# Kernel optimization log

Measured on AMD Instinct MI355X. Metric: run time of the kernel, lower is better.

The kernel has to match this reference:

```python
import jax, jax.numpy as jnp
import numpy as np

PROPAGATION_RANGE = 2
PROP_OUT = PROPAGATION_RANGE - 1  # propagation_out_range


def setup_inputs() -> dict:
    key = jax.random.key(0)
    k1, k2 = jax.random.split(key)
    B, D, H, W = 2, 48, 512, 640
    neighbors = 9
    depth_min = jnp.full((B,), 425.0, dtype=jnp.float32)
    depth_max = jnp.full((B,), 935.0, dtype=jnp.float32)
    # depth samples uniformly inside [depth_min, depth_max]
    u = jax.random.uniform(k1, (B, D, H, W), dtype=jnp.float32)
    depth_sample = depth_min[:, None, None, None] + u * (depth_max - depth_min)[:, None, None, None]
    # per-neighbor weights (2*neighbors channels: far-range then near-range)
    offset = jax.random.uniform(k2, (B, 2 * neighbors, H, W), dtype=jnp.float32) / neighbors
    return {
        "depth_sample": depth_sample,
        "depth_min": depth_min,
        "depth_max": depth_max,
        "offset": offset,
        "patchmatch_interval_scale": 0.025,
        "evaluate_neighbors": neighbors,
    }


def reference(depth_sample, depth_min, depth_max, offset, patchmatch_interval_scale, evaluate_neighbors):
    neighbors = int(evaluate_neighbors)
    B, D, H, W = depth_sample.shape
    k = int(np.sqrt(neighbors))  # square neighborhood side

    # normalized inverse depth in [0, 1]
    inv_min = 1.0 / depth_min  # [B]
    inv_max = 1.0 / depth_max  # [B]
    x = (1.0 / depth_sample - inv_max[:, None, None, None]) / (inv_min - inv_max)[:, None, None, None]

    pad = k // 2 + PROP_OUT
    pad1 = 2 * pad
    xp = jnp.pad(x, ((0, 0), (0, 0), (pad, pad), (pad, pad)), mode="reflect")
    xp1 = jnp.pad(x, ((0, 0), (0, 0), (pad1, pad1), (pad1, pad1)), mode="reflect")

    step = PROP_OUT + 1
    acc = jnp.zeros_like(x)
    for s in range(neighbors):  # small static loop (9 neighbors)
        iy, ix = (s // k) * step, (s % k) * step
        iy1, ix1 = 2 * iy, 2 * ix
        # offset channel broadcasts over the depth dimension
        f1 = offset[:, s, None] * xp1[:, :, iy1:H + iy1, ix1:W + ix1]
        f = offset[:, s + neighbors, None] * xp[:, :, iy:H + iy, ix:W + ix]
        acc = acc + (f + f1) * 0.5

    x1 = jnp.abs(acc - x) / patchmatch_interval_scale
    x1 = jnp.clip(x1, 0.0, 4.0)
    return jax.nn.sigmoid((2.0 - x1) * 2.0)
```

## Files before the change

### kernel.cpp

```cpp
#include <hip/hip_runtime.h>

constexpr int Bc = 2, Dc = 48, Hc = 512, Wc = 640;
constexpr int HWc = Hc * Wc;

constexpr int TW = 32, TH = 16, NT = 256;
constexpr int NXT = Wc / TW;
constexpr int NYT = Hc / TH;
constexpr int NBLK = NXT * NYT * Bc;
constexpr int NXCD = 8;
constexpr int BPX = NBLK / NXCD;
constexpr int HALO = 4;
constexpr int SW = TW + 2 * HALO;
constexpr int SH = TH + 2 * HALO;
constexpr int PLANE = SW * SH;
constexpr int DC = 4;
constexpr int NIT = Dc / DC;
constexpr int NVEC = DC * PLANE / 4;
constexpr int VPT = (NVEC + NT - 1) / NT;
constexpr int NSC = DC * PLANE;
constexpr int SPT = NSC / NT;

__device__ __forceinline__ int reflect_h(int h) {
    return h < 0 ? -h : (h >= Hc ? 2 * (Hc - 1) - h : h);
}
__device__ __forceinline__ int reflect_w(int w) {
    return w < 0 ? -w : (w >= Wc ? 2 * (Wc - 1) - w : w);
}

__global__ __launch_bounds__(NT) void dw_kernel(
    const float* __restrict__ ds, const float* __restrict__ dmin,
    const float* __restrict__ dmax, const float* __restrict__ off,
    const float* __restrict__ scale_p, float* __restrict__ out)
{
    __shared__ float sx[2][DC * PLANE];

    const int hw  = blockIdx.x;
    const int l   = (hw & (NXCD - 1)) * BPX + (hw >> 3);
    const int bx  = l % NXT;
    const int rem = l / NXT;
    const int by  = rem % NYT;
    const int b   = rem / NYT;
    const int h0  = by * TH;
    const int w0  = bx * TW;
    const int tid = threadIdx.x;
    const int col = tid & 15;
    const int row = tid >> 4;

    const float inv_min   = 1.0f / dmin[b];
    const float inv_max   = 1.0f / dmax[b];
    const float invd      = 1.0f / (inv_min - inv_max);
    const float nmc       = -inv_max * invd;
    const float inv_scale = 1.0f / scale_p[0];

    float offF[9][2], offN[9][2];
    {
        const float* op = off + (size_t)b * 18 * HWc
                        + (size_t)(h0 + row) * Wc + (w0 + 2 * col);
        #pragma unroll
        for (int s = 0; s < 9; ++s) {
            float2 vF = *(const float2*)(op + (size_t)s * HWc);
            float2 vN = *(const float2*)(op + (size_t)(s + 9) * HWc);
            offF[s][0] = 0.5f * vF.x; offF[s][1] = 0.5f * vF.y;
            offN[s][0] = 0.5f * vN.x; offN[s][1] = 0.5f * vN.y;
        }
    }

    const float* dsb  = ds  + (size_t)b * Dc * HWc;
    float*       outb = out + (size_t)b * Dc * HWc
                            + (size_t)(h0 + row) * Wc + (w0 + 2 * col);

    auto compute = [&](const float* sb, int d0) {
        #pragma unroll
        for (int p = 0; p < DC; ++p) {
            const float* bp = sb + p * PLANE + (row + HALO) * SW + (HALO + 2 * col);
            float a0 = 0.f, a1 = 0.f, x00, x01;
            float2 t0, t1, t2, t3, t4;
            t0 = *(const float2*)(bp - 4 * SW - 4);
            t1 = *(const float2*)(bp - 4 * SW);
            t2 = *(const float2*)(bp - 4 * SW + 4);
            a0 += offF[0][0]*t0.x + offF[1][0]*t1.x + offF[2][0]*t2.x;
            a1 += offF[0][1]*t0.y + offF[1][1]*t1.y + offF[2][1]*t2.y;
            t0 = *(const float2*)(bp - 2 * SW - 2);
            t1 = *(const float2*)(bp - 2 * SW);
            t2 = *(const float2*)(bp - 2 * SW + 2);
            a0 += offN[0][0]*t0.x + offN[1][0]*t1.x + offN[2][0]*t2.x;
            a1 += offN[0][1]*t0.y + offN[1][1]*t1.y + offN[2][1]*t2.y;
            t0 = *(const float2*)(bp - 4);
            t1 = *(const float2*)(bp - 2);
            t2 = *(const float2*)(bp);
            t3 = *(const float2*)(bp + 2);
            t4 = *(const float2*)(bp + 4);
            x00 = t2.x; x01 = t2.y;
            a0 += offN[3][0]*t1.x + offN[4][0]*t2.x + offN[5][0]*t3.x
                + offF[3][0]*t0.x + offF[4][0]*t2.x + offF[5][0]*t4.x;
            a1 += offN[3][1]*t1.y + offN[4][1]*t2.y + offN[5][1]*t3.y
                + offF[3][1]*t0.y + offF[4][1]*t2.y + offF[5][1]*t4.y;
            t0 = *(const float2*)(bp + 2 * SW - 2);
            t1 = *(const float2*)(bp + 2 * SW);
            t2 = *(const float2*)(bp + 2 * SW + 2);
            a0 += offN[6][0]*t0.x + offN[7][0]*t1.x + offN[8][0]*t2.x;
            a1 += offN[6][1]*t0.y + offN[7][1]*t1.y + offN[8][1]*t2.y;
            t0 = *(const float2*)(bp + 4 * SW - 4);
            t1 = *(const float2*)(bp + 4 * SW);
            t2 = *(const float2*)(bp + 4 * SW + 4);
            a0 += offF[6][0]*t0.x + offF[7][0]*t1.x + offF[8][0]*t2.x;
            a1 += offF[6][1]*t0.y + offF[7][1]*t1.y + offF[8][1]*t2.y;
            float2 o;
            float x1a = fminf(fabsf(a0 - x00) * inv_scale, 4.0f);
            float x1b = fminf(fabsf(a1 - x01) * inv_scale, 4.0f);
            o.x = __builtin_amdgcn_rcpf(1.0f + __expf(-(4.0f - 2.0f * x1a)));
            o.y = __builtin_amdgcn_rcpf(1.0f + __expf(-(4.0f - 2.0f * x1b)));
            *(float2*)(outb + (size_t)(d0 + p) * HWc) = o;
        }
    };

    const bool interior = (bx > 0) && (bx + 1 < NXT);

    if (interior) {
        int vsrc[VPT];
        #pragma unroll
        for (int i = 0; i < VPT; ++i) {
            int vid = tid + i * NT;
            if (vid < NVEC) {
                int p    = vid / (PLANE / 4);
                int rem2 = vid - p * (PLANE / 4);
                int r    = rem2 / (SW / 4);
                int j    = rem2 - r * (SW / 4);
                int hs   = reflect_h(h0 + r - HALO);
                vsrc[i]  = p * HWc + hs * Wc + (w0 - HALO + 4 * j);
            } else vsrc[i] = 0;
        }
        float4 pre[VPT];
        auto issue = [&](int d0) {
            const float* dp = dsb + (size_t)d0 * HWc;
            #pragma unroll
            for (int i = 0; i < VPT; ++i) {
                int vid = tid + i * NT;
                if (vid < NVEC) pre[i] = *(const float4*)(dp + vsrc[i]);
            }
        };
        auto commit = [&](float* sb) {
            #pragma unroll
            for (int i = 0; i < VPT; ++i) {
                int vid = tid + i * NT;
                if (vid < NVEC) {
                    float4 v = pre[i], x;
                    x.x = fmaf(__builtin_amdgcn_rcpf(v.x), invd, nmc);
                    x.y = fmaf(__builtin_amdgcn_rcpf(v.y), invd, nmc);
                    x.z = fmaf(__builtin_amdgcn_rcpf(v.z), invd, nmc);
                    x.w = fmaf(__builtin_amdgcn_rcpf(v.w), invd, nmc);
                    *(float4*)(sb + vid * 4) = x;
                }
            }
        };
        issue(0);
        commit(sx[0]);
        __syncthreads();
        for (int it = 0; it < NIT; ++it) {
            if (it + 1 < NIT) issue((it + 1) * DC);
            compute(sx[it & 1], it * DC);
            if (it + 1 < NIT) commit(sx[(it + 1) & 1]);
            __syncthreads();
        }
    } else {
        auto stage_direct = [&](int d0, float* sb) {
            const float* dp = dsb + (size_t)d0 * HWc;
            #pragma unroll
            for (int c = 0; c < 2; ++c) {
                const int kn = (c == 0) ? 8 : (SPT - 8);
                int adr[8]; float val[8];
                #pragma unroll
                for (int i = 0; i < 8; ++i) {
                    if (i < kn) {
                        int idx  = tid + (c * 8 + i) * NT;
                        int p    = idx / PLANE;
                        int rem2 = idx - p * PLANE;
                        int r    = rem2 / SW;
                        int cc   = rem2 - r * SW;
                        int hs   = reflect_h(h0 + r - HALO);
                        int ws   = reflect_w(w0 + cc - HALO);
                        adr[i]   = p * HWc + hs * Wc + ws;
                    }
                }
                #pragma unroll
                for (int i = 0; i < 8; ++i)
                    if (i < kn) val[i] = dp[adr[i]];
                #pragma unroll
                for (int i = 0; i < 8; ++i)
                    if (i < kn) {
                        int idx = tid + (c * 8 + i) * NT;
                        sb[idx] = fmaf(__builtin_amdgcn_rcpf(val[i]), invd, nmc);
                    }
            }
        };
        stage_direct(0, sx[0]);
        __syncthreads();
        for (int it = 0; it < NIT; ++it) {
            compute(sx[it & 1], it * DC);
            if (it + 1 < NIT) stage_direct((it + 1) * DC, sx[(it + 1) & 1]);
            __syncthreads();
        }
    }
}

extern "C" void kernel_launch(void* const* d_in, const int* in_sizes, int n_in,
                              void* d_out, int out_size, void* d_ws, size_t ws_size,
                              hipStream_t stream) {
    const float* ds   = (const float*)d_in[0];
    const float* dmin = (const float*)d_in[1];
    const float* dmax = (const float*)d_in[2];
    const float* off  = (const float*)d_in[3];
    const float* sc   = (const float*)d_in[4];
    float* out = (float*)d_out;

    dim3 grid(NBLK, 1, 1);
    dw_kernel<<<grid, NT, 0, stream>>>(ds, dmin, dmax, off, sc, out);
}
```

Measured before the change: 286.8 us.

## Deepen register prefetch to two stages, halve depth chunk, unify edge path

Each stage now covers two depth planes instead of four, and two register prefetch buffers keep loads two iterations ahead. The separate scalar-load path for edge tiles is removed: all tiles use float4 loads, with per-element reflect only for vectors that cross the image border. The full __syncthreads is replaced by an LDS-only waitcnt plus s_barrier, so outstanding global loads can stay in flight across the barrier. The aim is to hide global latency better and cut LDS use for higher occupancy, at the cost of more barriers and more registers for the extra prefetch buffer.

```diff
diff --git a/kernel.cpp b/kernel.cpp
--- a/kernel.cpp
+++ b/kernel.cpp
@@ -13,12 +13,10 @@
 constexpr int SW = TW + 2 * HALO;
 constexpr int SH = TH + 2 * HALO;
 constexpr int PLANE = SW * SH;
-constexpr int DC = 4;
+constexpr int DC = 2;
 constexpr int NIT = Dc / DC;
 constexpr int NVEC = DC * PLANE / 4;
 constexpr int VPT = (NVEC + NT - 1) / NT;
-constexpr int NSC = DC * PLANE;
-constexpr int SPT = NSC / NT;
 
 __device__ __forceinline__ int reflect_h(int h) {
     return h < 0 ? -h : (h >= Hc ? 2 * (Hc - 1) - h : h);
@@ -69,7 +67,65 @@
     float*       outb = out + (size_t)b * Dc * HWc
                             + (size_t)(h0 + row) * Wc + (w0 + 2 * col);
 
-    auto compute = [&](const float* sb, int d0) {
+    int vsrc[VPT], vcol[VPT];
+    #pragma unroll
+    for (int i = 0; i < VPT; ++i) {
+        int vid = tid + i * NT;
+        if (vid < NVEC) {
+            int p    = vid / (PLANE / 4);
+            int rem2 = vid - p * (PLANE / 4);
+            int r    = rem2 / (SW / 4);
+            int j    = rem2 - r * (SW / 4);
+            int hs   = reflect_h(h0 + r - HALO);
+            vsrc[i]  = p * HWc + hs * Wc;
+            vcol[i]  = w0 - HALO + 4 * j;
+        } else { vsrc[i] = 0; vcol[i] = 0; }
+    }
+
+    float4 pA[VPT], pB[VPT];
+
+    auto issue = [&](float4* pre, int iv) {
+        const float* dp = dsb + (size_t)(iv * DC) * HWc;
+        #pragma unroll
+        for (int i = 0; i < VPT; ++i) {
+            int vid = tid + i * NT;
+            if (vid < NVEC) {
+                const float* rp = dp + vsrc[i];
+                int c0 = vcol[i];
+                if (c0 >= 0 && c0 + 4 <= Wc) {
+                    pre[i] = *(const float4*)(rp + c0);
+                } else {
+                    float4 v;
+                    v.x = rp[reflect_w(c0)];
+                    v.y = rp[reflect_w(c0 + 1)];
+                    v.z = rp[reflect_w(c0 + 2)];
+                    v.w = rp[reflect_w(c0 + 3)];
+                    pre[i] = v;
+                }
+            }
+        }
+    };
+    auto commit = [&](const float4* pre, float* sb) {
+        #pragma unroll
+        for (int i = 0; i < VPT; ++i) {
+            int vid = tid + i * NT;
+            if (vid < NVEC) {
+                float4 v = pre[i], x;
+                x.x = fmaf(__builtin_amdgcn_rcpf(v.x), invd, nmc);
+                x.y = fmaf(__builtin_amdgcn_rcpf(v.y), invd, nmc);
+                x.z = fmaf(__builtin_amdgcn_rcpf(v.z), invd, nmc);
+                x.w = fmaf(__builtin_amdgcn_rcpf(v.w), invd, nmc);
+                *(float4*)(sb + vid * 4) = x;
+            }
+        }
+    };
+
+    auto bar = [&]() {
+        asm volatile("s_waitcnt lgkmcnt(0)" ::: "memory");
+        __builtin_amdgcn_s_barrier();
+    };
+
+    auto compute = [&](const float* sb, int iv) {
         #pragma unroll
         for (int p = 0; p < DC; ++p) {
             const float* bp = sb + p * PLANE + (row + HALO) * SW + (HALO + 2 * col);
@@ -110,96 +166,23 @@
             float x1b = fminf(fabsf(a1 - x01) * inv_scale, 4.0f);
             o.x = __builtin_amdgcn_rcpf(1.0f + __expf(-(4.0f - 2.0f * x1a)));
             o.y = __builtin_amdgcn_rcpf(1.0f + __expf(-(4.0f - 2.0f * x1b)));
-            *(float2*)(outb + (size_t)(d0 + p) * HWc) = o;
-        }
-    };
-
-    const bool interior = (bx > 0) && (bx + 1 < NXT);
-
-    if (interior) {
-        int vsrc[VPT];
-        #pragma unroll
-        for (int i = 0; i < VPT; ++i) {
-            int vid = tid + i * NT;
-            if (vid < NVEC) {
-                int p    = vid / (PLANE / 4);
-                int rem2 = vid - p * (PLANE / 4);
-                int r    = rem2 / (SW / 4);
-                int j    = rem2 - r * (SW / 4);
-                int hs   = reflect_h(h0 + r - HALO);
-                vsrc[i]  = p * HWc + hs * Wc + (w0 - HALO + 4 * j);
-            } else vsrc[i] = 0;
-        }
-        float4 pre[VPT];
-        auto issue = [&](int d0) {
-            const float* dp = dsb + (size_t)d0 * HWc;
-            #pragma unroll
-            for (int i = 0; i < VPT; ++i) {
-                int vid = tid + i * NT;
-                if (vid < NVEC) pre[i] = *(const float4*)(dp + vsrc[i]);
-            }
-        };
-        auto commit = [&](float* sb) {
-            #pragma unroll
-            for (int i = 0; i < VPT; ++i) {
-                int vid = tid + i * NT;
-                if (vid < NVEC) {
-                    float4 v = pre[i], x;
-                    x.x = fmaf(__builtin_amdgcn_rcpf(v.x), invd, nmc);
-                    x.y = fmaf(__builtin_amdgcn_rcpf(v.y), invd, nmc);
-                    x.z = fmaf(__builtin_amdgcn_rcpf(v.z), invd, nmc);
-                    x.w = fmaf(__builtin_amdgcn_rcpf(v.w), invd, nmc);
-                    *(float4*)(sb + vid * 4) = x;
-                }
-            }
-        };
-        issue(0);
-        commit(sx[0]);
-        __syncthreads();
-        for (int it = 0; it < NIT; ++it) {
-            if (it + 1 < NIT) issue((it + 1) * DC);
-            compute(sx[it & 1], it * DC);
-            if (it + 1 < NIT) commit(sx[(it + 1) & 1]);
-            __syncthreads();
-        }
-    } else {
-        auto stage_direct = [&](int d0, float* sb) {
-            const float* dp = dsb + (size_t)d0 * HWc;
-            #pragma unroll
-            for (int c = 0; c < 2; ++c) {
-                const int kn = (c == 0) ? 8 : (SPT - 8);
-                int adr[8]; float val[8];
-                #pragma unroll
-                for (int i = 0; i < 8; ++i) {
-                    if (i < kn) {
-                        int idx  = tid + (c * 8 + i) * NT;
-                        int p    = idx / PLANE;
-                        int rem2 = idx - p * PLANE;
-                        int r    = rem2 / SW;
-                        int cc   = rem2 - r * SW;
-                        int hs   = reflect_h(h0 + r - HALO);
-                        int ws   = reflect_w(w0 + cc - HALO);
-                        adr[i]   = p * HWc + hs * Wc + ws;
-                    }
-                }
-                #pragma unroll
-                for (int i = 0; i < 8; ++i)
-                    if (i < kn) val[i] = dp[adr[i]];
-                #pragma unroll
-                for (int i = 0; i < 8; ++i)
-                    if (i < kn) {
-                        int idx = tid + (c * 8 + i) * NT;
-                        sb[idx] = fmaf(__builtin_amdgcn_rcpf(val[i]), invd, nmc);
-                    }
-            }
-        };
-        stage_direct(0, sx[0]);
-        __syncthreads();
-        for (int it = 0; it < NIT; ++it) {
-            compute(sx[it & 1], it * DC);
-            if (it + 1 < NIT) stage_direct((it + 1) * DC, sx[(it + 1) & 1]);
-            __syncthreads();
-        }
+            *(float2*)(outb + (size_t)(iv * DC + p) * HWc) = o;
+        }
+    };
+
+    issue(pA, 0);
+    commit(pA, sx[0]);
+    issue(pA, 1);
+    bar();
+    for (int it = 0; it < NIT; it += 2) {
+        if (it + 2 < NIT) issue(pB, it + 2);
+        compute(sx[0], it);
+        commit(pA, sx[1]);
+        bar();
+        if (it + 3 < NIT) issue(pA, it + 3);
+        compute(sx[1], it + 1);
+        if (it + 2 < NIT) commit(pB, sx[0]);
+        bar();
     }
 }
 
```

Result: slower. 292.9 us (+2.1%).
